# Kernel tuning notes

Hardware: AMD Instinct MI355X
Metric: run time of the kernel (lower is better)

Reference implementation:

```python
import jax, jax.numpy as jnp
import numpy as np

JITTER = 1e-6
LOG_2PI_BASE = 2.0 * np.pi  # multiplied by sigma_sq inside log


def rbf_kernel(x1, x2, lengthscale, outputscale):
    """gpytorch ScaleKernel(RBFKernel): outputscale * exp(-0.5 * ||(x1-x2)/ls||^2)."""
    x1s = x1 / lengthscale
    x2s = x2 / lengthscale
    sq = (jnp.sum(x1s * x1s, axis=1)[:, None]
          + jnp.sum(x2s * x2s, axis=1)[None, :]
          - 2.0 * (x1s @ x2s.T))
    sq = jnp.maximum(sq, 0.0)
    return outputscale * jnp.exp(-0.5 * sq)


def setup_inputs() -> dict:
    key = jax.random.key(0)
    k = jax.random.split(key, 4)
    n, m, d = 8192, 512, 8
    return {
        "train_x": jax.random.normal(k[0], (n, d), dtype=jnp.float32),
        "train_y": jax.random.normal(k[1], (n,), dtype=jnp.float32),
        "inducing_points": jax.random.normal(k[2], (m, d), dtype=jnp.float32),
        "q_mu": jnp.zeros((m, 1), dtype=jnp.float32),
        "q_log_var": jnp.eye(m, dtype=jnp.float32),
        "likelihood_log_variance": jnp.asarray(0.0, dtype=jnp.float32),
        "lengthscale": jnp.asarray(1.0, dtype=jnp.float32),
        "outputscale": jnp.asarray(1.0, dtype=jnp.float32),
    }


def reference(train_x, train_y, inducing_points, q_mu, q_log_var,
              likelihood_log_variance, lengthscale, outputscale):
    n = train_x.shape[0]
    m = inducing_points.shape[0]
    eye_m = jnp.eye(m, dtype=train_x.dtype)

    # --- predict(train_x): q(f) = N(pred_mean, pred_cov) ---
    K_ff = rbf_kernel(train_x, train_x, lengthscale, outputscale)          # [n, n]
    K_uu = rbf_kernel(inducing_points, inducing_points, lengthscale, outputscale) + JITTER * eye_m
    K_uf = rbf_kernel(inducing_points, train_x, lengthscale, outputscale)  # [m, n]

    L_uu = jnp.linalg.cholesky(K_uu)                                       # lower [m, m]
    Lam = jax.scipy.linalg.solve_triangular(L_uu, K_uf, lower=True)        # [m, n]
    pred_mean = (Lam.T @ q_mu)[:, 0]                                       # [n]

    q_sqrt = jnp.tril(jnp.exp(0.5 * q_log_var))                            # [m, m]
    q_cov = q_sqrt @ q_sqrt.T + JITTER * eye_m                             # [m, m]

    S = K_ff - Lam.T @ Lam                                                 # [n, n]
    V = Lam.T @ q_cov                                                      # [n, m]
    pred_cov = S + V @ V.T                                                 # [n, n]

    # --- expected log likelihood E_{q(f)}[log N(y | f, sigma^2 I)] / n ---
    sigma_sq = jnp.exp(likelihood_log_variance)
    diff = train_y - pred_mean
    ell = jnp.sum(-0.5 * (diff * diff + jnp.diagonal(pred_cov)) / sigma_sq
                  - 0.5 * jnp.log(LOG_2PI_BASE * sigma_sq)) / n

    # --- KL( N(q_mu, q_cov) || N(0, I) ) / n ---
    Lq = jnp.linalg.cholesky(q_cov)
    logdet_q = 2.0 * jnp.sum(jnp.log(jnp.diagonal(Lq)))
    mu = q_mu[:, 0]
    kl = 0.5 * (jnp.trace(q_cov) + mu @ mu - m - logdet_q) / n

    return ell - kl
```

## Files before the change

### kernel.cpp

```cpp
#include <hip/hip_runtime.h>
#include <math.h>

#define MI 512
#define NPT 8192
#define JIT 1e-6f
#define LOG2PI 1.8378770664093453f

#define OFF_A     0
#define OFF_LINV  262144
#define OFF_QS    524288
#define OFF_QC    786432
#define OFF_DINV  1048576
#define OFF_PART  1081856
#define OFF_FLAGS 1082368
#define NFLAGS 211

#define FMA16(ACC,a0,a1,a2,a3,b0,b1,b2,b3) \
  ACC[0][0]+=a0*b0; ACC[0][1]+=a0*b1; ACC[0][2]+=a0*b2; ACC[0][3]+=a0*b3; \
  ACC[1][0]+=a1*b0; ACC[1][1]+=a1*b1; ACC[1][2]+=a1*b2; ACC[1][3]+=a1*b3; \
  ACC[2][0]+=a2*b0; ACC[2][1]+=a2*b1; ACC[2][2]+=a2*b2; ACC[2][3]+=a2*b3; \
  ACC[3][0]+=a3*b0; ACC[3][1]+=a3*b1; ACC[3][2]+=a3*b2; ACC[3][3]+=a3*b3;

__device__ __forceinline__ void wait_flag(unsigned* f, int tid) {
  if (tid == 0) {
    while (__hip_atomic_load(f, __ATOMIC_RELAXED, __HIP_MEMORY_SCOPE_AGENT) == 0)
      __builtin_amdgcn_s_sleep(2);
    __builtin_amdgcn_fence(__ATOMIC_ACQUIRE, "agent");
  }
  __syncthreads();
}
__device__ __forceinline__ void wait_count(unsigned* c, unsigned tgt, int tid) {
  if (tid == 0) {
    while (__hip_atomic_load(c, __ATOMIC_RELAXED, __HIP_MEMORY_SCOPE_AGENT) < tgt)
      __builtin_amdgcn_s_sleep(2);
    __builtin_amdgcn_fence(__ATOMIC_ACQUIRE, "agent");
  }
  __syncthreads();
}
__device__ __forceinline__ void raise_flag(unsigned* f, int tid) {
  __syncthreads();
  if (tid == 0) {
    __builtin_amdgcn_fence(__ATOMIC_RELEASE, "agent");
    __hip_atomic_store(f, 1u, __ATOMIC_RELAXED, __HIP_MEMORY_SCOPE_AGENT);
  }
}
__device__ __forceinline__ void publish_tile(unsigned* f, unsigned* cnt, int tid) {
  __syncthreads();
  if (tid == 0) {
    __builtin_amdgcn_fence(__ATOMIC_RELEASE, "agent");
    __hip_atomic_store(f, 1u, __ATOMIC_RELAXED, __HIP_MEMORY_SCOPE_AGENT);
    __hip_atomic_fetch_add(cnt, 1u, __ATOMIC_RELAXED, __HIP_MEMORY_SCOPE_AGENT);
  }
}

__global__ __launch_bounds__(256) void k_prep(const float* __restrict__ Z,
    const float* __restrict__ qlv, const float* __restrict__ lsP,
    const float* __restrict__ osP, float* __restrict__ ws) {
  int u = blockIdx.x*256 + threadIdx.x;
  if (blockIdx.x < 27) {
    int fi = blockIdx.x*256 + threadIdx.x;
    if (fi < NFLAGS*32) ((unsigned*)(ws + OFF_FLAGS))[fi] = 0u;
  }
  float ls = lsP[0], os = osP[0];
  float ils2 = 1.0f/(ls*ls);
  if (u < MI*MI) {
    int i = u >> 9, j = u & 511;
    float4 a0 = *(const float4*)(Z + i*8);
    float4 a1 = *(const float4*)(Z + i*8 + 4);
    float4 b0 = *(const float4*)(Z + j*8);
    float4 b1 = *(const float4*)(Z + j*8 + 4);
    float d0=a0.x-b0.x, d1=a0.y-b0.y, d2=a0.z-b0.z, d3=a0.w-b0.w;
    float d4=a1.x-b1.x, d5=a1.y-b1.y, d6=a1.z-b1.z, d7=a1.w-b1.w;
    float sq = d0*d0+d1*d1+d2*d2+d3*d3+d4*d4+d5*d5+d6*d6+d7*d7;
    float v = os*__expf(-0.5f*ils2*sq);
    if (i==j) v += JIT;
    ws[OFF_A + u] = v;
  } else {
    int w2 = u - MI*MI;
    if (w2 < MI*MI) {
      int i = w2 >> 9, j = w2 & 511;
      ws[OFF_QS + w2] = (j <= i) ? __expf(0.5f*qlv[w2]) : 0.0f;
    }
  }
}

__global__ __launch_bounds__(256, 3) void k_dag(const float* __restrict__ X,
    const float* __restrict__ Yv, const float* __restrict__ Z,
    const float* __restrict__ qmu, const float* __restrict__ qlv,
    const float* __restrict__ llvP, const float* __restrict__ lsP,
    const float* __restrict__ osP, float* __restrict__ ws,
    float* __restrict__ out) {
  __shared__ float SH[13340];
  float* A    = ws + OFF_A;
  float* LT   = ws + OFF_LINV;
  const float* QC = ws + OFF_QC;
  float* DINV = ws + OFF_DINV;
  float* PART = ws + OFF_PART;
  unsigned* FB = (unsigned*)(ws + OFF_FLAGS);
  #define FLA(i) (FB + (i)*32)
  int bid = blockIdx.x, tid = threadIdx.x;
  int ty4 = (tid >> 4)*4, tx4 = (tid & 15)*4;

  if (bid < 8) {
    __builtin_amdgcn_s_setprio(3);
    int b = bid, Rb = b*64;
    float* Dg = SH;
    float* Sa = SH + 4160;
    float* Sb = SH + 8320;
    float* TMP = SH + 12480;
    for (int e = tid; e < 4096; e += 256)
      Dg[(e>>6)*65 + (e&63)] = A[(Rb + (e>>6))*512 + Rb + (e&63)];

    for (int p = 0; p < b; ++p) {
      if (p > 0) wait_flag(FLA(144 + b*8 + p), tid);
      for (int e = tid; e < 4096; e += 256)
        Sb[(e>>6)*65 + (e&63)] = A[(Rb + (e>>6))*512 + p*64 + (e&63)];
      wait_flag(FLA(p), tid);
      for (int e = tid; e < 4096; e += 256)
        Sa[(e>>6)*65 + (e&63)] = DINV[p*4096 + e];
      __syncthreads();
      float acc2[4][4] = {{0.f}};
      for (int m = 0; m < 64; ++m) {
        float a0=Sb[(ty4+0)*65+m],a1=Sb[(ty4+1)*65+m],a2=Sb[(ty4+2)*65+m],a3=Sb[(ty4+3)*65+m];
        float b0=Sa[(tx4+0)*65+m],b1=Sa[(tx4+1)*65+m],b2=Sa[(tx4+2)*65+m],b3=Sa[(tx4+3)*65+m];
        FMA16(acc2,a0,a1,a2,a3,b0,b1,b2,b3)
      }
      __syncthreads();
      #pragma unroll
      for (int u = 0; u < 4; ++u)
        #pragma unroll
        for (int v = 0; v < 4; ++v) {
          Sb[(ty4+u)*65 + tx4+v] = acc2[u][v];
          A[(Rb+ty4+u)*512 + p*64 + tx4+v] = acc2[u][v];
        }
      raise_flag(FLA(8 + b*8 + p), tid);
      float c2[4][4] = {{0.f}};
      for (int m = 0; m < 64; ++m) {
        float a0=Sb[(ty4+0)*65+m],a1=Sb[(ty4+1)*65+m],a2=Sb[(ty4+2)*65+m],a3=Sb[(ty4+3)*65+m];
        float b0=Sb[(tx4+0)*65+m],b1=Sb[(tx4+1)*65+m],b2=Sb[(tx4+2)*65+m],b3=Sb[(tx4+3)*65+m];
        FMA16(c2,a0,a1,a2,a3,b0,b1,b2,b3)
      }
      #pragma unroll
      for (int u = 0; u < 4; ++u)
        #pragma unroll
        for (int v = 0; v < 4; ++v)
          Dg[(ty4+u)*65 + tx4+v] -= c2[u][v];
    }
    __syncthreads();

    for (int e = tid; e < 4096; e += 256) Sa[(e>>6)*65 + (e&63)] = 0.0f;
    __syncthreads();
    for (int t = 0; t < 4; ++t) {
      const int c0 = t*16;
      if (tid < 16) {
        float a[16];
        #pragma unroll
        for (int j = 0; j < 16; ++j) a[j] = Dg[(c0+tid)*65 + c0 + j];
        float rr = 0.f;
        #pragma unroll
        for (int j = 0; j < 16; ++j) {
          float d = __shfl(a[j], j);
          float r = rsqrtf(d);
          r = r*(1.5f - 0.5f*d*r*r);
          if (tid == j) rr = r;
          a[j] *= r;
          #pragma unroll
          for (int k = j+1; k < 16; ++k)
            a[k] -= a[j]*__shfl(a[j], k);
        }
        #pragma unroll
        for (int j = 0; j < 16; ++j)
          Dg[(c0+tid)*65 + c0 + j] = (j <= tid) ? a[j] : 0.0f;
        float v[16];
        #pragma unroll
        for (int i = 0; i < 16; ++i) {
          float s = (tid == i) ? 1.0f : 0.0f;
          #pragma unroll
          for (int k = 0; k < i; ++k)
            s -= Dg[(c0+i)*65 + c0 + k]*v[k];
          v[i] = s * __shfl(rr, i);
        }
        #pragma unroll
        for (int i = 0; i < 16; ++i)
          Sa[(c0+i)*65 + c0 + tid] = v[i];
      }
      __syncthreads();
      if (t < 3) {
        const int cnt = 48 - c0;
        const int r0 = c0 + 16;
        float res[3];
        int nout = cnt*16, idx = 0;
        for (int e = tid; e < nout; e += 256, ++idx) {
          int r = r0 + (e >> 4), j = e & 15;
          float s = 0.f;
          #pragma unroll
          for (int m = 0; m < 16; ++m)
            s += Dg[r*65 + c0 + m]*Sa[(c0+j)*65 + c0 + m];
          res[idx] = s;
        }
        __syncthreads();
        idx = 0;
        for (int e = tid; e < nout; e += 256, ++idx)
          Dg[(r0 + (e >> 4))*65 + c0 + (e & 15)] = res[idx];
        __syncthreads();
        for (int e = tid; e < cnt*cnt; e += 256) {
          int r = r0 + e/cnt, c = r0 + e%cnt;
          float s = 0.f;
          #pragma unroll
          for (int m = 0; m < 16; ++m)
            s += Dg[r*65 + c0 + m]*Dg[c*65 + c0 + m];
          Dg[r*65 + c] -= s;
        }
        __syncthreads();
      }
    }
    for (int d = 1; d < 4; ++d) {
      int nout = (4-d)*256;
      for (int e = tid; e < nout; e += 256) {
        int bs = e >> 8, I = bs, J = I + d;
        int i = (e >> 4) & 15, c = e & 15;
        float s = 0.f;
        for (int k = I; k < J; ++k) {
          #pragma unroll
          for (int m = 0; m < 16; ++m)
            s += Dg[(J*16+i)*65 + k*16+m]*Sa[(k*16+m)*65 + I*16+c];
        }
        TMP[bs*272 + i*17 + c] = s;
      }
      __syncthreads();
      for (int e = tid; e < nout; e += 256) {
        int bs = e >> 8, I = bs, J = I + d;
        int i = (e >> 4) & 15, c = e & 15;
        float s = 0.f;
        #pragma unroll
        for (int m = 0; m < 16; ++m)
          s += Sa[(J*16+i)*65 + J*16+m]*TMP[bs*272 + m*17 + c];
        Sa[(J*16+i)*65 + I*16+c] = -s;
      }
      __syncthreads();
    }
    for (int e = tid; e < 4096; e += 256)
      DINV[b*4096 + e] = Sa[(e>>6)*65 + (e&63)];
    raise_flag(FLA(b), tid);
    return;
  }

  if (bid < 44) {
    __builtin_amdgcn_s_setprio(2);
    int t = bid - 8;
    int s = 0, rem = t;
    while (rem >= s+1) { rem -= (s+1); ++s; }
    int J = rem;
    if (s == J) {
      wait_flag(FLA(s), tid);
      for (int e = tid; e < 4096; e += 256) {
        int i = e >> 6, j = e & 63;
        LT[(64*s+j)*512 + 64*s + i] = DINV[s*4096 + e];
      }
      publish_tile(FLA(72 + s*8 + J), FLA(136 + s), tid);
      return;
    }
    float* Ls = SH;
    float* Vs = SH + 4160;
    float* T  = SH + 8320;
    float acc[4][4] = {{0.f}};
    for (int k = J; k < s; ++k) {
      wait_flag(FLA(72 + k*8 + J), tid);
      wait_flag(FLA(8 + s*8 + k), tid);
      for (int e = tid; e < 1024; e += 256) {
        int row = e >> 4, m4 = (e & 15)*4;
        float4 a = *(const float4*)(A + (64*s+row)*512 + 64*k + m4);
        Ls[row*65+m4+0]=a.x; Ls[row*65+m4+1]=a.y; Ls[row*65+m4+2]=a.z; Ls[row*65+m4+3]=a.w;
        float4 v = *(const float4*)(LT + (64*J+row)*512 + 64*k + m4);
        Vs[(m4+0)*65+row]=v.x; Vs[(m4+1)*65+row]=v.y; Vs[(m4+2)*65+row]=v.z; Vs[(m4+3)*65+row]=v.w;
      }
      __syncthreads();
      for (int m = 0; m < 64; ++m) {
        float a0=Ls[(ty4+0)*65+m],a1=Ls[(ty4+1)*65+m],a2=Ls[(ty4+2)*65+m],a3=Ls[(ty4+3)*65+m];
        float b0=Vs[m*65+tx4+0],b1=Vs[m*65+tx4+1],b2=Vs[m*65+tx4+2],b3=Vs[m*65+tx4+3];
        FMA16(acc,a0,a1,a2,a3,b0,b1,b2,b3)
      }
      __syncthreads();
    }
    wait_flag(FLA(s), tid);
    #pragma unroll
    for (int u = 0; u < 4; ++u)
      #pragma unroll
      for (int v = 0; v < 4; ++v)
        T[(ty4+u)*65 + tx4+v] = acc[u][v];
    for (int e = tid; e < 4096; e += 256) Ls[(e>>6)*65 + (e&63)] = DINV[s*4096 + e];
    __syncthreads();
    float acc2[4][4] = {{0.f}};
    for (int m = 0; m < 64; ++m) {
      float a0=Ls[(ty4+0)*65+m],a1=Ls[(ty4+1)*65+m],a2=Ls[(ty4+2)*65+m],a3=Ls[(ty4+3)*65+m];
      float b0=T[m*65+tx4+0],b1=T[m*65+tx4+1],b2=T[m*65+tx4+2],b3=T[m*65+tx4+3];
      FMA16(acc2,a0,a1,a2,a3,b0,b1,b2,b3)
    }
    #pragma unroll
    for (int u = 0; u < 4; ++u)
      #pragma unroll
      for (int v = 0; v < 4; ++v)
        LT[(64*J+tx4+v)*512 + 64*s+ty4+u] = -acc2[u][v];
    publish_tile(FLA(72 + s*8 + J), FLA(136 + s), tid);
    return;
  }

  if (bid < 65) {
    __builtin_amdgcn_s_setprio(2);
    int hid = bid - 44;
    int b = 2, rem = hid;
    while (rem >= b-1) { rem -= (b-1); ++b; }
    int p = rem + 1;
    float* Sa = SH;
    float* Sb = SH + 4160;
    float gacc[4][4] = {{0.f}};
    for (int pp = 0; pp < p; ++pp) {
      wait_flag(FLA(8 + b*8 + pp), tid);
      wait_flag(FLA(8 + p*8 + pp), tid);
      for (int e = tid; e < 4096; e += 256) {
        int row = e>>6, col = e&63;
        Sa[row*65+col] = A[(b*64+row)*512 + pp*64 + col];
        Sb[row*65+col] = A[(p*64+row)*512 + pp*64 + col];
      }
      __syncthreads();
      for (int m = 0; m < 64; ++m) {
        float a0=Sa[(ty4+0)*65+m],a1=Sa[(ty4+1)*65+m],a2=Sa[(ty4+2)*65+m],a3=Sa[(ty4+3)*65+m];
        float b0=Sb[(tx4+0)*65+m],b1=Sb[(tx4+1)*65+m],b2=Sb[(tx4+2)*65+m],b3=Sb[(tx4+3)*65+m];
        FMA16(gacc,a0,a1,a2,a3,b0,b1,b2,b3)
      }
      __syncthreads();
    }
    #pragma unroll
    for (int u = 0; u < 4; ++u)
      #pragma unroll
      for (int v = 0; v < 4; ++v)
        A[(b*64+ty4+u)*512 + p*64 + tx4+v] -= gacc[u][v];
    raise_flag(FLA(144 + b*8 + p), tid);
    return;
  }

  if (bid < 129) {
    __builtin_amdgcn_s_setprio(1);
    int cid = bid - 65;
    int bi = cid >> 3, bj = cid & 7;
    const float* QSp = ws + OFF_QS;
    float* QCw = ws + OFF_QC;
    float* Xs2 = SH;
    float* Ys2 = SH + 1280;
    int lrow = tid >> 2, lc4 = (tid & 3)*4;
    float acc[4][4] = {{0.f}};
    for (int kc = 0; kc < 512; kc += 16) {
      float4 xa = *(const float4*)(QSp + (bi*64+lrow)*512 + kc + lc4);
      float4 ya = *(const float4*)(QSp + (bj*64+lrow)*512 + kc + lc4);
      Xs2[lrow*20+lc4+0]=xa.x; Xs2[lrow*20+lc4+1]=xa.y; Xs2[lrow*20+lc4+2]=xa.z; Xs2[lrow*20+lc4+3]=xa.w;
      Ys2[lrow*20+lc4+0]=ya.x; Ys2[lrow*20+lc4+1]=ya.y; Ys2[lrow*20+lc4+2]=ya.z; Ys2[lrow*20+lc4+3]=ya.w;
      __syncthreads();
      #pragma unroll
      for (int kk = 0; kk < 16; ++kk) {
        float a0=Xs2[(ty4+0)*20+kk],a1=Xs2[(ty4+1)*20+kk],a2=Xs2[(ty4+2)*20+kk],a3=Xs2[(ty4+3)*20+kk];
        float b0=Ys2[(tx4+0)*20+kk],b1=Ys2[(tx4+1)*20+kk],b2=Ys2[(tx4+2)*20+kk],b3=Ys2[(tx4+3)*20+kk];
        FMA16(acc,a0,a1,a2,a3,b0,b1,b2,b3)
      }
      __syncthreads();
    }
    #pragma unroll
    for (int u = 0; u < 4; ++u)
      #pragma unroll
      for (int v = 0; v < 4; ++v) {
        int gi = bi*64+ty4+u, gj = bj*64+tx4+v;
        float o = acc[u][v]; if (gi==gj) o += JIT;
        QCw[gi*512+gj] = o;
      }
    __syncthreads();
    if (tid == 0) {
      __builtin_amdgcn_fence(__ATOMIC_RELEASE, "agent");
      __hip_atomic_fetch_add(FLA(208), 1u, __ATOMIC_RELAXED, __HIP_MEMORY_SCOPE_AGENT);
    }
    return;
  }

  {
    int B = bid - 129;
    float* KL  = SH;
    float* PB  = SH + 8192;
    float* FB2 = SH + 11456;
    float* qsh = SH + 12736;
    float* Xs  = SH + 8192;
    float* RD  = SH + 8192;
    float* elli= SH + 9824;
    int* lastf = (int*)(SH + 13248);
    float ls = lsP[0], os = osP[0], llv = llvP[0];
    float ils2 = 1.0f/(ls*ls);
    if (tid < 128) { int pp = tid>>3, d = tid&7; Xs[pp*8+d] = X[(B*16+pp)*8 + d]; }
    qsh[tid] = qmu[tid]; qsh[tid+256] = qmu[tid+256];
    __syncthreads();
    for (int e = tid; e < 8192; e += 256) {
      int cc = e >> 4, pp = e & 15;
      float4 z0 = *(const float4*)(Z + cc*8);
      float4 z1 = *(const float4*)(Z + cc*8 + 4);
      float d0=z0.x-Xs[pp*8+0], d1=z0.y-Xs[pp*8+1], d2=z0.z-Xs[pp*8+2], d3=z0.w-Xs[pp*8+3];
      float d4=z1.x-Xs[pp*8+4], d5=z1.y-Xs[pp*8+5], d6=z1.z-Xs[pp*8+6], d7=z1.w-Xs[pp*8+7];
      float sq = d0*d0+d1*d1+d2*d2+d3*d3+d4*d4+d5*d5+d6*d6+d7*d7;
      KL[e] = os*__expf(-0.5f*ils2*sq);
    }
    wait_count(FLA(208), 64u, tid);

    int gq = tid >> 6;
    int lr = (tid >> 2) & 15;
    int lrow4 = lr*4;
    int pq4 = (tid & 3)*4;
    int rq4 = (tid >> 2)*4;
    float pmp[4] = {0.f,0.f,0.f,0.f}, lsp[4] = {0.f,0.f,0.f,0.f};
    float ua0[4][4] = {{0.f}}, ua1[4][4] = {{0.f}};

    for (int s = 0; s < 8; ++s) {
      wait_count(FLA(136 + s), (unsigned)(s+1), tid);
      int Q = 16*(s+1);
      int cbeg = gq*Q, cend = cbeg + Q;
      float acc[4][4] = {{0.f}};
      const float* Lcol = LT + 64*s + lrow4;
      #pragma unroll 4
      for (int c = cbeg; c < cend; ++c) {
        float4 kv = *(const float4*)&KL[c*16 + pq4];
        float4 lv = *(const float4*)(Lcol + c*512);
        FMA16(acc, lv.x,lv.y,lv.z,lv.w, kv.x,kv.y,kv.z,kv.w)
      }
      if (gq > 0) {
        float* pb = PB + (gq-1)*1088;
        #pragma unroll
        for (int u = 0; u < 4; ++u)
          #pragma unroll
          for (int v = 0; v < 4; ++v)
            pb[(lrow4+u)*17 + pq4+v] = acc[u][v];
      }
      __syncthreads();
      if (gq == 0) {
        #pragma unroll
        for (int u = 0; u < 4; ++u) {
          float qv = qsh[64*s + lrow4 + u];
          #pragma unroll
          for (int v = 0; v < 4; ++v) {
            float f = acc[u][v]
                    + PB[(lrow4+u)*17 + pq4+v]
                    + PB[1088 + (lrow4+u)*17 + pq4+v]
                    + PB[2176 + (lrow4+u)*17 + pq4+v];
            FB2[(lrow4+u)*20 + pq4+v] = f;
            pmp[v] += f*qv;
            lsp[v] += f*f;
          }
        }
      }
      __syncthreads();
      #pragma unroll 2
      for (int cl = 0; cl < 64; ++cl) {
        float4 kv = *(const float4*)&FB2[cl*20 + pq4];
        float4 q0 = *(const float4*)(QC + (64*s+cl)*512 + rq4);
        float4 q1 = *(const float4*)(QC + (64*s+cl)*512 + 256 + rq4);
        FMA16(ua0, q0.x,q0.y,q0.z,q0.w, kv.x,kv.y,kv.z,kv.w)
        FMA16(ua1, q1.x,q1.y,q1.z,q1.w, kv.x,kv.y,kv.z,kv.w)
      }
    }
    __syncthreads();

    if (gq == 0) {
      #pragma unroll
      for (int v = 0; v < 4; ++v) {
        RD[lr*17 + pq4+v] = pmp[v];
        RD[272 + lr*17 + pq4+v] = lsp[v];
      }
    }
    float usq[4] = {0.f,0.f,0.f,0.f};
    #pragma unroll
    for (int u = 0; u < 4; ++u)
      #pragma unroll
      for (int v = 0; v < 4; ++v)
        usq[v] += ua0[u][v]*ua0[u][v] + ua1[u][v]*ua1[u][v];
    #pragma unroll
    for (int v = 0; v < 4; ++v)
      RD[544 + (tid>>2)*17 + pq4+v] = usq[v];
    __syncthreads();
    if (tid < 16) {
      float pm = 0.f, lq = 0.f, us = 0.f;
      for (int r2 = 0; r2 < 16; ++r2) {
        pm += RD[r2*17 + tid];
        lq += RD[272 + r2*17 + tid];
      }
      for (int r2 = 0; r2 < 64; ++r2)
        us += RD[544 + r2*17 + tid];
      int gi = B*16 + tid;
      float diff = Yv[gi] - pm;
      float diagc = os + us - lq;
      float iss = __expf(-llv);
      elli[tid] = -0.5f*((diff*diff + diagc)*iss + (LOG2PI + llv));
    }
    __syncthreads();
    if (tid == 0) {
      float sum = 0.f;
      #pragma unroll
      for (int i2 = 0; i2 < 16; ++i2) sum += elli[i2];
      PART[B] = sum;
      __builtin_amdgcn_fence(__ATOMIC_RELEASE, "agent");
      unsigned old = __hip_atomic_fetch_add(FLA(209), 1u, __ATOMIC_RELAXED, __HIP_MEMORY_SCOPE_AGENT);
      lastf[0] = (old == 511u) ? 1 : 0;
    }
    __syncthreads();
    if (lastf[0]) {
      if (tid == 0) __builtin_amdgcn_fence(__ATOMIC_ACQUIRE, "agent");
      __syncthreads();
      double* sh = (double*)SH;
      double pa = 0.0, tr = 0.0, mm = 0.0, ld = 0.0;
      for (int i = tid; i < 512; i += 256) {
        pa += (double)PART[i];
        tr += (double)QC[i*513];
        double q = (double)qmu[i]; mm += q*q;
        ld += (double)qlv[i*513];
      }
      double vals[4] = {pa, tr, mm, ld};
      double res[4];
      for (int t2 = 0; t2 < 4; ++t2) {
        sh[tid] = vals[t2]; __syncthreads();
        for (int s2 = 128; s2 > 0; s2 >>= 1) {
          if (tid < s2) sh[tid] += sh[tid+s2];
          __syncthreads();
        }
        res[t2] = sh[0]; __syncthreads();
      }
      if (tid == 0) {
        double n = 8192.0;
        double ell = res[0]/n;
        double kl = 0.5*(res[1] + res[2] - 512.0 - res[3])/n;
        out[0] = (float)(ell - kl);
      }
    }
  }
}

extern "C" void kernel_launch(void* const* d_in, const int* in_sizes, int n_in,
                              void* d_out, int out_size, void* d_ws, size_t ws_size,
                              hipStream_t stream) {
  (void)in_sizes; (void)n_in; (void)out_size; (void)ws_size;
  const float* X   = (const float*)d_in[0];
  const float* Y   = (const float*)d_in[1];
  const float* Z   = (const float*)d_in[2];
  const float* qmu = (const float*)d_in[3];
  const float* qlv = (const float*)d_in[4];
  const float* llv = (const float*)d_in[5];
  const float* ls  = (const float*)d_in[6];
  const float* os  = (const float*)d_in[7];
  float* ws = (float*)d_ws;
  float* out = (float*)d_out;

  k_prep<<<2048, 256, 0, stream>>>(Z, qlv, ls, os, ws);
  k_dag<<<641, 256, 0, stream>>>(X, Y, Z, qmu, qlv, llv, ls, os, ws, out);
}
```

Before: 359.0 us.

## Replace agent-scope fences with coherent sc0/sc1 loads and stores in Cholesky pipeline

The inter-block flag protocol in the blocked Cholesky/inverse stages drops the release and acquire fences. In their place, producer stores and consumer loads of shared tiles use inline-asm global loads and stores with sc0 sc1 cache-coherence bits, plus explicit vmcnt waits. Tile copies are also vectorised to dwordx4. The aim is to avoid cache writeback and invalidate costs on the critical dependency chain. The risk is memory-ordering bugs wherever a path still uses plain loads (the LT reads, and wait_flag is kept in some places).

Result: faster. 344.8 us (-4.0%).

```diff
diff --git a/kernel.cpp b/kernel.cpp
--- a/kernel.cpp
+++ b/kernel.cpp
@@ -21,6 +21,29 @@
   ACC[2][0]+=a2*b0; ACC[2][1]+=a2*b1; ACC[2][2]+=a2*b2; ACC[2][3]+=a2*b3; \
   ACC[3][0]+=a3*b0; ACC[3][1]+=a3*b1; ACC[3][2]+=a3*b2; ACC[3][3]+=a3*b3;
 
+typedef float f4 __attribute__((ext_vector_type(4)));
+
+__device__ __forceinline__ f4 ld_coh(const float* p) {
+  f4 r;
+  asm volatile("global_load_dwordx4 %0, %1, off sc0 sc1\n\ts_waitcnt vmcnt(0)"
+               : "=v"(r) : "v"(p) : "memory");
+  return r;
+}
+__device__ __forceinline__ void ld_coh4x4(const float* p0, const float* p1,
+    const float* p2, const float* p3, f4& a, f4& b, f4& c, f4& d) {
+  asm volatile(
+    "global_load_dwordx4 %0, %4, off sc0 sc1\n\t"
+    "global_load_dwordx4 %1, %5, off sc0 sc1\n\t"
+    "global_load_dwordx4 %2, %6, off sc0 sc1\n\t"
+    "global_load_dwordx4 %3, %7, off sc0 sc1\n\t"
+    "s_waitcnt vmcnt(0)"
+    : "=&v"(a), "=&v"(b), "=&v"(c), "=&v"(d)
+    : "v"(p0), "v"(p1), "v"(p2), "v"(p3) : "memory");
+}
+__device__ __forceinline__ void st_coh(float* p, f4 v) {
+  asm volatile("global_store_dwordx4 %0, %1, off sc0 sc1" :: "v"(p), "v"(v) : "memory");
+}
+
 __device__ __forceinline__ void wait_flag(unsigned* f, int tid) {
   if (tid == 0) {
     while (__hip_atomic_load(f, __ATOMIC_RELAXED, __HIP_MEMORY_SCOPE_AGENT) == 0)
@@ -36,13 +59,6 @@
     __builtin_amdgcn_fence(__ATOMIC_ACQUIRE, "agent");
   }
   __syncthreads();
-}
-__device__ __forceinline__ void raise_flag(unsigned* f, int tid) {
-  __syncthreads();
-  if (tid == 0) {
-    __builtin_amdgcn_fence(__ATOMIC_RELEASE, "agent");
-    __hip_atomic_store(f, 1u, __ATOMIC_RELAXED, __HIP_MEMORY_SCOPE_AGENT);
-  }
 }
 __device__ __forceinline__ void publish_tile(unsigned* f, unsigned* cnt, int tid) {
   __syncthreads();
@@ -52,6 +68,21 @@
     __hip_atomic_fetch_add(cnt, 1u, __ATOMIC_RELAXED, __HIP_MEMORY_SCOPE_AGENT);
   }
 }
+__device__ __forceinline__ void wait_flag_nf(unsigned* f, int tid) {
+  if (tid == 0)
+    while (__hip_atomic_load(f, __ATOMIC_RELAXED, __HIP_MEMORY_SCOPE_AGENT) == 0)
+      __builtin_amdgcn_s_sleep(2);
+  __syncthreads();
+}
+__device__ __forceinline__ void raise_flag_nf(unsigned* f, int tid) {
+  asm volatile("s_waitcnt vmcnt(0)" ::: "memory");
+  __syncthreads();
+  if (tid == 0)
+    __hip_atomic_store(f, 1u, __ATOMIC_RELAXED, __HIP_MEMORY_SCOPE_AGENT);
+}
+
+#define SCAT65(Sdst, fi, gv) { int r_=(fi)>>4, c_=((fi)&15)*4; \
+  Sdst[r_*65+c_+0]=gv.x; Sdst[r_*65+c_+1]=gv.y; Sdst[r_*65+c_+2]=gv.z; Sdst[r_*65+c_+3]=gv.w; }
 
 __global__ __launch_bounds__(256) void k_prep(const float* __restrict__ Z,
     const float* __restrict__ qlv, const float* __restrict__ lsP,
@@ -112,12 +143,24 @@
       Dg[(e>>6)*65 + (e&63)] = A[(Rb + (e>>6))*512 + Rb + (e&63)];
 
     for (int p = 0; p < b; ++p) {
-      if (p > 0) wait_flag(FLA(144 + b*8 + p), tid);
-      for (int e = tid; e < 4096; e += 256)
-        Sb[(e>>6)*65 + (e&63)] = A[(Rb + (e>>6))*512 + p*64 + (e&63)];
-      wait_flag(FLA(p), tid);
-      for (int e = tid; e < 4096; e += 256)
-        Sa[(e>>6)*65 + (e&63)] = DINV[p*4096 + e];
+      if (p > 0) wait_flag_nf(FLA(144 + b*8 + p), tid);
+      {
+        int f0 = tid, f1 = tid+256, f2 = tid+512, f3 = tid+768;
+        f4 g0,g1,g2,g3;
+        ld_coh4x4(A + (Rb + (f0>>4))*512 + p*64 + (f0&15)*4,
+                  A + (Rb + (f1>>4))*512 + p*64 + (f1&15)*4,
+                  A + (Rb + (f2>>4))*512 + p*64 + (f2&15)*4,
+                  A + (Rb + (f3>>4))*512 + p*64 + (f3&15)*4, g0,g1,g2,g3);
+        SCAT65(Sb, f0, g0) SCAT65(Sb, f1, g1) SCAT65(Sb, f2, g2) SCAT65(Sb, f3, g3)
+      }
+      wait_flag_nf(FLA(p), tid);
+      {
+        int f0 = tid, f1 = tid+256, f2 = tid+512, f3 = tid+768;
+        f4 d0,d1,d2,d3;
+        ld_coh4x4(DINV + p*4096 + f0*4, DINV + p*4096 + f1*4,
+                  DINV + p*4096 + f2*4, DINV + p*4096 + f3*4, d0,d1,d2,d3);
+        SCAT65(Sa, f0, d0) SCAT65(Sa, f1, d1) SCAT65(Sa, f2, d2) SCAT65(Sa, f3, d3)
+      }
       __syncthreads();
       float acc2[4][4] = {{0.f}};
       for (int m = 0; m < 64; ++m) {
@@ -127,13 +170,15 @@
       }
       __syncthreads();
       #pragma unroll
-      for (int u = 0; u < 4; ++u)
-        #pragma unroll
-        for (int v = 0; v < 4; ++v) {
-          Sb[(ty4+u)*65 + tx4+v] = acc2[u][v];
-          A[(Rb+ty4+u)*512 + p*64 + tx4+v] = acc2[u][v];
-        }
-      raise_flag(FLA(8 + b*8 + p), tid);
+      for (int u = 0; u < 4; ++u) {
+        f4 lv = {acc2[u][0], acc2[u][1], acc2[u][2], acc2[u][3]};
+        st_coh(A + (Rb+ty4+u)*512 + p*64 + tx4, lv);
+        Sb[(ty4+u)*65 + tx4+0] = acc2[u][0];
+        Sb[(ty4+u)*65 + tx4+1] = acc2[u][1];
+        Sb[(ty4+u)*65 + tx4+2] = acc2[u][2];
+        Sb[(ty4+u)*65 + tx4+3] = acc2[u][3];
+      }
+      raise_flag_nf(FLA(8 + b*8 + p), tid);
       float c2[4][4] = {{0.f}};
       for (int m = 0; m < 64; ++m) {
         float a0=Sb[(ty4+0)*65+m],a1=Sb[(ty4+1)*65+m],a2=Sb[(ty4+2)*65+m],a3=Sb[(ty4+3)*65+m];
@@ -239,9 +284,13 @@
       }
       __syncthreads();
     }
-    for (int e = tid; e < 4096; e += 256)
-      DINV[b*4096 + e] = Sa[(e>>6)*65 + (e&63)];
-    raise_flag(FLA(b), tid);
+    #pragma unroll
+    for (int kk = 0; kk < 4; ++kk) {
+      int fi = tid + kk*256; int r_ = fi>>4, c_ = (fi&15)*4;
+      f4 dv = {Sa[r_*65+c_+0], Sa[r_*65+c_+1], Sa[r_*65+c_+2], Sa[r_*65+c_+3]};
+      st_coh(DINV + b*4096 + fi*4, dv);
+    }
+    raise_flag_nf(FLA(b), tid);
     return;
   }
 
@@ -252,10 +301,16 @@
     while (rem >= s+1) { rem -= (s+1); ++s; }
     int J = rem;
     if (s == J) {
-      wait_flag(FLA(s), tid);
-      for (int e = tid; e < 4096; e += 256) {
-        int i = e >> 6, j = e & 63;
-        LT[(64*s+j)*512 + 64*s + i] = DINV[s*4096 + e];
+      wait_flag_nf(FLA(s), tid);
+      {
+        int f0 = tid, f1 = tid+256, f2 = tid+512, f3 = tid+768;
+        f4 d0,d1,d2,d3;
+        ld_coh4x4(DINV + s*4096 + f0*4, DINV + s*4096 + f1*4,
+                  DINV + s*4096 + f2*4, DINV + s*4096 + f3*4, d0,d1,d2,d3);
+        #define LTW(fi, dv) { int i_=(fi)>>4, j_=((fi)&15)*4; \
+          LT[(64*s+j_+0)*512+64*s+i_]=dv.x; LT[(64*s+j_+1)*512+64*s+i_]=dv.y; \
+          LT[(64*s+j_+2)*512+64*s+i_]=dv.z; LT[(64*s+j_+3)*512+64*s+i_]=dv.w; }
+        LTW(f0, d0) LTW(f1, d1) LTW(f2, d2) LTW(f3, d3)
       }
       publish_tile(FLA(72 + s*8 + J), FLA(136 + s), tid);
       return;
@@ -266,13 +321,19 @@
     float acc[4][4] = {{0.f}};
     for (int k = J; k < s; ++k) {
       wait_flag(FLA(72 + k*8 + J), tid);
-      wait_flag(FLA(8 + s*8 + k), tid);
-      for (int e = tid; e < 1024; e += 256) {
-        int row = e >> 4, m4 = (e & 15)*4;
-        float4 a = *(const float4*)(A + (64*s+row)*512 + 64*k + m4);
-        Ls[row*65+m4+0]=a.x; Ls[row*65+m4+1]=a.y; Ls[row*65+m4+2]=a.z; Ls[row*65+m4+3]=a.w;
-        float4 v = *(const float4*)(LT + (64*J+row)*512 + 64*k + m4);
-        Vs[(m4+0)*65+row]=v.x; Vs[(m4+1)*65+row]=v.y; Vs[(m4+2)*65+row]=v.z; Vs[(m4+3)*65+row]=v.w;
+      wait_flag_nf(FLA(8 + s*8 + k), tid);
+      {
+        int f0 = tid, f1 = tid+256, f2 = tid+512, f3 = tid+768;
+        f4 a0,a1,a2,a3;
+        ld_coh4x4(A + (64*s+(f0>>4))*512 + 64*k + (f0&15)*4,
+                  A + (64*s+(f1>>4))*512 + 64*k + (f1&15)*4,
+                  A + (64*s+(f2>>4))*512 + 64*k + (f2&15)*4,
+                  A + (64*s+(f3>>4))*512 + 64*k + (f3&15)*4, a0,a1,a2,a3);
+        #define LSV(fi, av) { int row=(fi)>>4, m4=((fi)&15)*4; \
+          Ls[row*65+m4+0]=av.x; Ls[row*65+m4+1]=av.y; Ls[row*65+m4+2]=av.z; Ls[row*65+m4+3]=av.w; \
+          float4 v = *(const float4*)(LT + (64*J+row)*512 + 64*k + m4); \
+          Vs[(m4+0)*65+row]=v.x; Vs[(m4+1)*65+row]=v.y; Vs[(m4+2)*65+row]=v.z; Vs[(m4+3)*65+row]=v.w; }
+        LSV(f0, a0) LSV(f1, a1) LSV(f2, a2) LSV(f3, a3)
       }
       __syncthreads();
       for (int m = 0; m < 64; ++m) {
@@ -282,13 +343,19 @@
       }
       __syncthreads();
     }
-    wait_flag(FLA(s), tid);
+    wait_flag_nf(FLA(s), tid);
     #pragma unroll
     for (int u = 0; u < 4; ++u)
       #pragma unroll
       for (int v = 0; v < 4; ++v)
         T[(ty4+u)*65 + tx4+v] = acc[u][v];
-    for (int e = tid; e < 4096; e += 256) Ls[(e>>6)*65 + (e&63)] = DINV[s*4096 + e];
+    {
+      int f0 = tid, f1 = tid+256, f2 = tid+512, f3 = tid+768;
+      f4 d0,d1,d2,d3;
+      ld_coh4x4(DINV + s*4096 + f0*4, DINV + s*4096 + f1*4,
+                DINV + s*4096 + f2*4, DINV + s*4096 + f3*4, d0,d1,d2,d3);
+      SCAT65(Ls, f0, d0) SCAT65(Ls, f1, d1) SCAT65(Ls, f2, d2) SCAT65(Ls, f3, d3)
+    }
     __syncthreads();
     float acc2[4][4] = {{0.f}};
     for (int m = 0; m < 64; ++m) {
@@ -315,12 +382,21 @@
     float* Sb = SH + 4160;
     float gacc[4][4] = {{0.f}};
     for (int pp = 0; pp < p; ++pp) {
-      wait_flag(FLA(8 + b*8 + pp), tid);
-      wait_flag(FLA(8 + p*8 + pp), tid);
-      for (int e = tid; e < 4096; e += 256) {
-        int row = e>>6, col = e&63;
-        Sa[row*65+col] = A[(b*64+row)*512 + pp*64 + col];
-        Sb[row*65+col] = A[(p*64+row)*512 + pp*64 + col];
+      wait_flag_nf(FLA(8 + b*8 + pp), tid);
+      wait_flag_nf(FLA(8 + p*8 + pp), tid);
+      {
+        int f0 = tid, f1 = tid+256, f2 = tid+512, f3 = tid+768;
+        f4 a0,a1,a2,a3, b0,b1,b2,b3;
+        ld_coh4x4(A + (b*64+(f0>>4))*512 + pp*64 + (f0&15)*4,
+                  A + (b*64+(f1>>4))*512 + pp*64 + (f1&15)*4,
+                  A + (b*64+(f2>>4))*512 + pp*64 + (f2&15)*4,
+                  A + (b*64+(f3>>4))*512 + pp*64 + (f3&15)*4, a0,a1,a2,a3);
+        ld_coh4x4(A + (p*64+(f0>>4))*512 + pp*64 + (f0&15)*4,
+                  A + (p*64+(f1>>4))*512 + pp*64 + (f1&15)*4,
+                  A + (p*64+(f2>>4))*512 + pp*64 + (f2&15)*4,
+                  A + (p*64+(f3>>4))*512 + pp*64 + (f3&15)*4, b0,b1,b2,b3);
+        SCAT65(Sa, f0, a0) SCAT65(Sa, f1, a1) SCAT65(Sa, f2, a2) SCAT65(Sa, f3, a3)
+        SCAT65(Sb, f0, b0) SCAT65(Sb, f1, b1) SCAT65(Sb, f2, b2) SCAT65(Sb, f3, b3)
       }
       __syncthreads();
       for (int m = 0; m < 64; ++m) {
@@ -330,12 +406,20 @@
       }
       __syncthreads();
     }
-    #pragma unroll
-    for (int u = 0; u < 4; ++u)
-      #pragma unroll
-      for (int v = 0; v < 4; ++v)
-        A[(b*64+ty4+u)*512 + p*64 + tx4+v] -= gacc[u][v];
-    raise_flag(FLA(144 + b*8 + p), tid);
+    {
+      float* r0 = A + (b*64+ty4+0)*512 + p*64 + tx4;
+      float* r1 = A + (b*64+ty4+1)*512 + p*64 + tx4;
+      float* r2 = A + (b*64+ty4+2)*512 + p*64 + tx4;
+      float* r3 = A + (b*64+ty4+3)*512 + p*64 + tx4;
+      f4 o0,o1,o2,o3;
+      ld_coh4x4(r0, r1, r2, r3, o0,o1,o2,o3);
+      f4 n0 = {o0.x-gacc[0][0], o0.y-gacc[0][1], o0.z-gacc[0][2], o0.w-gacc[0][3]};
+      f4 n1 = {o1.x-gacc[1][0], o1.y-gacc[1][1], o1.z-gacc[1][2], o1.w-gacc[1][3]};
+      f4 n2 = {o2.x-gacc[2][0], o2.y-gacc[2][1], o2.z-gacc[2][2], o2.w-gacc[2][3]};
+      f4 n3 = {o3.x-gacc[3][0], o3.y-gacc[3][1], o3.z-gacc[3][2], o3.w-gacc[3][3]};
+      st_coh(r0, n0); st_coh(r1, n1); st_coh(r2, n2); st_coh(r3, n3);
+    }
+    raise_flag_nf(FLA(144 + b*8 + p), tid);
     return;
   }
 
```
